# Optimization experiments

Measured on AMD Instinct MI355X. Metric: run time of the kernel, lower is better.

## Reference

```python
import jax, jax.numpy as jnp
import numpy as np

S = 8192          # past KV length
H = 4096          # hidden size
NH = 32           # heads
HD = 128          # head dim
INNER = 16384     # MLP inner (4h)
ROT = 64          # rotary dim per 2D-rope half
NUM_LAYERS = 28
LAYER_ID = 0
ALPHA = (2.0 * NUM_LAYERS) ** 0.5
QK_COEFF = float(LAYER_ID + 1)            # query_key_layer_scaling_coeff
COEFF = (128.0 ** 0.5) * QK_COEFF         # math.sqrt(128) * coeff
EPS = 1e-5


def layernorm(x, w, b):
    mu = jnp.mean(x, axis=-1, keepdims=True)
    var = jnp.var(x, axis=-1, keepdims=True)
    return (x - mu) * jax.lax.rsqrt(var + EPS) * w + b


def rotate_half(x):
    # x: [..., 64]; GLM rotate-half at 32
    return jnp.concatenate([-x[..., 32:], x[..., :32]], axis=-1)


def setup_inputs() -> dict:
    key = jax.random.key(0)
    ks = jax.random.split(key, 16)
    # rotary cache (as in the driver script)
    inv_freq = 1.0 / (10000.0 ** (jnp.arange(0, ROT, 2, dtype=jnp.float32) / ROT))  # [32]
    t = jnp.arange(512, dtype=jnp.float32)
    freqs = jnp.einsum('i,j->ij', t, inv_freq)          # [512,32]
    emb = jnp.concatenate([freqs, freqs], axis=-1)      # [512,64]
    w = lambda k, shp: jax.random.normal(k, shp, dtype=jnp.float32) * 0.02
    return {
        'hidden_states': jax.random.normal(ks[0], (1, H), dtype=jnp.float32),
        'past_key': jax.random.normal(ks[1], (S, NH, HD), dtype=jnp.float32),
        'past_value': jax.random.normal(ks[2], (S, NH, HD), dtype=jnp.float32),
        'cos_cached': jnp.cos(emb),
        'sin_cached': jnp.sin(emb),
        'ln1_w': jnp.ones((H,), jnp.float32), 'ln1_b': jnp.zeros((H,), jnp.float32),
        'qkv_w': w(ks[3], (3 * H, H)), 'qkv_b': w(ks[4], (3 * H,)),
        'dense_w': w(ks[5], (H, H)), 'dense_b': w(ks[6], (H,)),
        'ln2_w': jnp.ones((H,), jnp.float32), 'ln2_b': jnp.zeros((H,), jnp.float32),
        'fc1_w': w(ks[7], (INNER, H)), 'fc1_b': w(ks[8], (INNER,)),
        'fc2_w': w(ks[9], (H, INNER)), 'fc2_b': w(ks[10], (H,)),
        'position_ids': jax.random.randint(ks[11], (1, 1), 0, 512),
        'block_position_ids': jax.random.randint(ks[12], (1, 1), 0, 512),
        'attention_mask': jnp.zeros((1, 1, S + 1), dtype=bool),
    }


def reference(hidden_states, past_key, past_value, cos_cached, sin_cached,
              ln1_w, ln1_b, qkv_w, qkv_b, dense_w, dense_b,
              ln2_w, ln2_b, fc1_w, fc1_b, fc2_w, fc2_b,
              position_ids, block_position_ids, attention_mask):
    # rotary lookups: embedding then transpose(0,1) -> [q_len,1,64]
    pos_cos = jnp.transpose(cos_cached[position_ids], (1, 0, 2))
    pos_sin = jnp.transpose(sin_cached[position_ids], (1, 0, 2))
    blk_cos = jnp.transpose(cos_cached[block_position_ids], (1, 0, 2))
    blk_sin = jnp.transpose(sin_cached[block_position_ids], (1, 0, 2))

    residual = layernorm(hidden_states, ln1_w, ln1_b)          # [1, H]
    qkv = residual @ qkv_w.T + qkv_b                           # [1, 3H]
    qkv = qkv.reshape(-1, NH, 3 * HD)                          # [1, 32, 384]
    query, key_new, value_new = jnp.split(qkv, 3, axis=2)      # each [1,32,128]

    q1, q2 = jnp.split(query, 2, axis=2)                       # [1,32,64] each
    k1, k2 = jnp.split(key_new, 2, axis=2)
    q1 = q1 * pos_cos + rotate_half(q1) * pos_sin
    k1 = k1 * pos_cos + rotate_half(k1) * pos_sin
    q2 = q2 * blk_cos + rotate_half(q2) * blk_sin
    k2 = k2 * blk_cos + rotate_half(k2) * blk_sin
    q = jnp.concatenate([q1, q2], axis=-1)                     # [1,32,128]
    k_new = jnp.concatenate([k1, k2], axis=-1)                 # [1,32,128]

    k = jnp.concatenate([past_key, k_new], axis=0)             # [S+1,32,128]
    v = jnp.concatenate([past_value, value_new], axis=0)       # [S+1,32,128]

    # scores: [heads, q=1, S+1]
    scores = jnp.einsum('qhd,khd->hqk', q / COEFF, k)
    scores = jnp.where(attention_mask, jnp.float32(-10000.0), scores)
    scores = scores * QK_COEFF
    probs = jax.nn.softmax(scores, axis=-1)
    ctx = jnp.einsum('hqk,khd->qhd', probs, v).reshape(-1, H)  # [1,4096]

    attn_out = ctx @ dense_w.T + dense_b
    hidden = residual * ALPHA + attn_out

    residual2 = layernorm(hidden, ln2_w, ln2_b)
    mlp = jax.nn.gelu(residual2 @ fc1_w.T + fc1_b, approximate=True)
    mlp = mlp @ fc2_w.T + fc2_b
    out = residual2 * ALPHA + mlp
    return (out, k, v)
```

## Files before the change

### kernel.cpp

```cpp
#include <hip/hip_runtime.h>
#include <math.h>

#define S_PAST 8192
#define S_TOT  8193
#define HID    4096
#define NH     32
#define HD     128
#define INNER  16384
#define CH     16
#define NCH    512
#define S_PAD  8224
#define ALPHA_ 7.483314773547883f
#define INV_COEFF 0.08838834764831845f
#define EPS_ 1e-5f

__global__ __launch_bounds__(256) void ln_kernel(const float* __restrict__ xin,
                                                 const float* __restrict__ w,
                                                 const float* __restrict__ b,
                                                 float* __restrict__ out) {
    int tid = threadIdx.x;
    float xs[16];
    float s = 0.f, s2 = 0.f;
#pragma unroll
    for (int i = 0; i < 16; ++i) {
        float v = xin[tid + i * 256];
        xs[i] = v; s += v; s2 += v * v;
    }
    for (int off = 32; off; off >>= 1) {
        s  += __shfl_down(s, off, 64);
        s2 += __shfl_down(s2, off, 64);
    }
    __shared__ float rs[4], rs2[4];
    __shared__ float mu_s, ri_s;
    int wid = tid >> 6, lane = tid & 63;
    if (lane == 0) { rs[wid] = s; rs2[wid] = s2; }
    __syncthreads();
    if (tid == 0) {
        float S1 = rs[0] + rs[1] + rs[2] + rs[3];
        float S2 = rs2[0] + rs2[1] + rs2[2] + rs2[3];
        float mu = S1 / HID;
        float var = S2 / HID - mu * mu;
        mu_s = mu;
        ri_s = rsqrtf(var + EPS_);
    }
    __syncthreads();
    float mu = mu_s, ri = ri_s;
#pragma unroll
    for (int i = 0; i < 16; ++i) {
        int idx = tid + i * 256;
        out[idx] = (xs[i] - mu) * ri * w[idx] + b[idx];
    }
}

template <int C, int MODE>
__global__ __launch_bounds__(256) void gemv_kernel(
        const float* __restrict__ Wm, const float* __restrict__ bias,
        const float* __restrict__ x, float* __restrict__ y,
        const float* __restrict__ res) {
    int wid = threadIdx.x >> 6, lane = threadIdx.x & 63;
    int r = blockIdx.x * 4 + wid;
    const float4* __restrict__ rowv = (const float4*)(Wm + (size_t)r * C);
    const float4* __restrict__ xv = (const float4*)x;
    constexpr int IT = C / 4 / 64;
    float acc0 = 0.f, acc1 = 0.f;
#pragma unroll
    for (int it = 0; it < IT; it += 2) {
        float4 w0 = rowv[lane + it * 64];
        float4 x0 = xv[lane + it * 64];
        float4 w1 = rowv[lane + (it + 1) * 64];
        float4 x1 = xv[lane + (it + 1) * 64];
        acc0 += w0.x * x0.x + w0.y * x0.y + w0.z * x0.z + w0.w * x0.w;
        acc1 += w1.x * x1.x + w1.y * x1.y + w1.z * x1.z + w1.w * x1.w;
    }
    float acc = acc0 + acc1;
    for (int off = 32; off; off >>= 1) acc += __shfl_down(acc, off, 64);
    if (lane == 0) {
        float t = acc + bias[r];
        if (MODE == 1) t += ALPHA_ * res[r];
        if (MODE == 2) {
            float u = t;
            t = 0.5f * u * (1.f + tanhf(0.7978845608028654f * (u + 0.044715f * u * u * u)));
        }
        y[r] = t;
    }
}

__global__ __launch_bounds__(128) void rope_kv_kernel(
        const float* __restrict__ qkv, const float* __restrict__ cosc,
        const float* __restrict__ sinc, const int* __restrict__ pos_ids,
        const int* __restrict__ blk_ids, float* __restrict__ qrot,
        float* __restrict__ kout, float* __restrict__ vout) {
    int h = blockIdx.x, d = threadIdx.x;
    int pos = pos_ids[0], blk = blk_ids[0];
    const float* qh = qkv + h * 384;
    float q = qh[d], k = qh[128 + d], v = qh[256 + d];
    int half = d >> 6;
    int i = d & 63;
    int p = half ? blk : pos;
    float c = cosc[p * 64 + i];
    float s = sinc[p * 64 + i];
    float qpart, kpart;
    int base = half * 64;
    if (i < 32) { qpart = -qh[base + i + 32]; kpart = -qh[128 + base + i + 32]; }
    else        { qpart =  qh[base + i - 32]; kpart =  qh[128 + base + i - 32]; }
    float qo = q * c + qpart * s;
    float ko = k * c + kpart * s;
    qrot[h * HD + d] = qo * INV_COEFF;
    size_t o = (size_t)S_PAST * HID + h * HD + d;
    kout[o] = ko;
    vout[o] = v;
}

__global__ __launch_bounds__(512) void scores_kcopy(
        const float* __restrict__ qrot, const float* __restrict__ pastk,
        float* __restrict__ kout, const unsigned char* __restrict__ mask,
        float* __restrict__ probs, float* __restrict__ pL) {
    int tid = threadIdx.x;
    int t = tid & 255, u = tid >> 8;
    int s0 = blockIdx.x * CH;
    int rows = (blockIdx.x == NCH - 1) ? (S_TOT - s0) : CH;
    int rstart = u * 8;
    int rend = u ? rows : 8;
    int a = t >> 5;
    const float4* __restrict__ qv = (const float4*)qrot;
    float4 q0 = qv[t], q1 = qv[256 + t], q2 = qv[512 + t], q3 = qv[768 + t];
    __shared__ float sc[CH + 1][NH + 1];
#pragma unroll 4
    for (int r = rstart; r < rend; ++r) {
        int srow = s0 + r;
        const float* kbase = (srow < S_PAST) ? pastk : kout;
        const float4* krow = (const float4*)(kbase + (size_t)srow * HID);
        float4 k0 = krow[t], k1 = krow[256 + t];
        float4 k2 = krow[512 + t], k3 = krow[768 + t];
        if (srow < S_PAST) {
            float4* ko = (float4*)(kout + (size_t)srow * HID);
            ko[t] = k0; ko[256 + t] = k1; ko[512 + t] = k2; ko[768 + t] = k3;
        }
        float d0 = q0.x * k0.x + q0.y * k0.y + q0.z * k0.z + q0.w * k0.w;
        float d1 = q1.x * k1.x + q1.y * k1.y + q1.z * k1.z + q1.w * k1.w;
        float d2 = q2.x * k2.x + q2.y * k2.y + q2.z * k2.z + q2.w * k2.w;
        float d3 = q3.x * k3.x + q3.y * k3.y + q3.z * k3.z + q3.w * k3.w;
#pragma unroll
        for (int off = 1; off < 32; off <<= 1) {
            d0 += __shfl_xor(d0, off, 64);
            d1 += __shfl_xor(d1, off, 64);
            d2 += __shfl_xor(d2, off, 64);
            d3 += __shfl_xor(d3, off, 64);
        }
        if ((t & 31) == 0) {
            if (mask[srow]) { d0 = d1 = d2 = d3 = -10000.f; }
            sc[r][a]      = __expf(d0);
            sc[r][8 + a]  = __expf(d1);
            sc[r][16 + a] = __expf(d2);
            sc[r][24 + a] = __expf(d3);
        }
    }
    __syncthreads();
    for (int i = tid; i < rows * NH; i += 512) {
        int h = i & 31, r = i >> 5;
        probs[(size_t)h * S_PAD + s0 + r] = sc[r][h];
    }
    if (tid < 256) {
        int h = tid >> 3, j = tid & 7;
        float e = 0.f;
        for (int r = j; r < rows; r += 8) e += sc[r][h];
#pragma unroll
        for (int off = 1; off < 8; off <<= 1) e += __shfl_xor(e, off, 64);
        if (j == 0) pL[h * NCH + blockIdx.x] = e;
    }
}

__global__ __launch_bounds__(512) void pv_vcopy(
        const float* __restrict__ probs, const float* __restrict__ pastv,
        float* __restrict__ vout, float* __restrict__ pctx) {
    int tid = threadIdx.x;
    int t = tid & 255, u = tid >> 8;
    int s0 = blockIdx.x * CH;
    int rows = (blockIdx.x == NCH - 1) ? (S_TOT - s0) : CH;
    int rstart = u * 8;
    int rend = u ? rows : 8;
    int a = t >> 5;
    __shared__ float pl[NH][CH + 2];
    __shared__ float acc_lds[256][16];
    for (int i = tid; i < rows * NH; i += 512) {
        int h = i & 31, r = i >> 5;
        pl[h][r] = probs[(size_t)h * S_PAD + s0 + r];
    }
    __syncthreads();
    float4 a0 = {0,0,0,0}, a1 = {0,0,0,0}, a2 = {0,0,0,0}, a3 = {0,0,0,0};
#pragma unroll 4
    for (int r = rstart; r < rend; ++r) {
        int srow = s0 + r;
        const float* vbase = (srow < S_PAST) ? pastv : vout;
        const float4* vrow = (const float4*)(vbase + (size_t)srow * HID);
        float4 v0 = vrow[t], v1 = vrow[256 + t];
        float4 v2 = vrow[512 + t], v3 = vrow[768 + t];
        if (srow < S_PAST) {
            float4* vo = (float4*)(vout + (size_t)srow * HID);
            vo[t] = v0; vo[256 + t] = v1; vo[512 + t] = v2; vo[768 + t] = v3;
        }
        float p0 = pl[a][r], p1 = pl[8 + a][r], p2 = pl[16 + a][r], p3 = pl[24 + a][r];
        a0.x += p0 * v0.x; a0.y += p0 * v0.y; a0.z += p0 * v0.z; a0.w += p0 * v0.w;
        a1.x += p1 * v1.x; a1.y += p1 * v1.y; a1.z += p1 * v1.z; a1.w += p1 * v1.w;
        a2.x += p2 * v2.x; a2.y += p2 * v2.y; a2.z += p2 * v2.z; a2.w += p2 * v2.w;
        a3.x += p3 * v3.x; a3.y += p3 * v3.y; a3.z += p3 * v3.z; a3.w += p3 * v3.w;
    }
    if (u == 1) {
        acc_lds[t][0]  = a0.x; acc_lds[t][1]  = a0.y; acc_lds[t][2]  = a0.z; acc_lds[t][3]  = a0.w;
        acc_lds[t][4]  = a1.x; acc_lds[t][5]  = a1.y; acc_lds[t][6]  = a1.z; acc_lds[t][7]  = a1.w;
        acc_lds[t][8]  = a2.x; acc_lds[t][9]  = a2.y; acc_lds[t][10] = a2.z; acc_lds[t][11] = a2.w;
        acc_lds[t][12] = a3.x; acc_lds[t][13] = a3.y; acc_lds[t][14] = a3.z; acc_lds[t][15] = a3.w;
    }
    __syncthreads();
    if (u == 0) {
        a0.x += acc_lds[t][0];  a0.y += acc_lds[t][1];  a0.z += acc_lds[t][2];  a0.w += acc_lds[t][3];
        a1.x += acc_lds[t][4];  a1.y += acc_lds[t][5];  a1.z += acc_lds[t][6];  a1.w += acc_lds[t][7];
        a2.x += acc_lds[t][8];  a2.y += acc_lds[t][9];  a2.z += acc_lds[t][10]; a2.w += acc_lds[t][11];
        a3.x += acc_lds[t][12]; a3.y += acc_lds[t][13]; a3.z += acc_lds[t][14]; a3.w += acc_lds[t][15];
        float4* pc = (float4*)(pctx + (size_t)blockIdx.x * HID);
        pc[t] = a0; pc[256 + t] = a1; pc[512 + t] = a2; pc[768 + t] = a3;
    }
}

__global__ __launch_bounds__(256) void ctx_reduce1(const float* __restrict__ pctx,
                                                   const float* __restrict__ pL,
                                                   float* __restrict__ pctx2,
                                                   float* __restrict__ pL2) {
    int b = blockIdx.x, tid = threadIdx.x;
    float4 a0 = {0,0,0,0}, a1 = {0,0,0,0}, a2 = {0,0,0,0}, a3 = {0,0,0,0};
#pragma unroll
    for (int c = 0; c < 8; ++c) {
        const float4* row = (const float4*)(pctx + (size_t)(b * 8 + c) * HID);
        float4 v0 = row[tid], v1 = row[256 + tid], v2 = row[512 + tid], v3 = row[768 + tid];
        a0.x += v0.x; a0.y += v0.y; a0.z += v0.z; a0.w += v0.w;
        a1.x += v1.x; a1.y += v1.y; a1.z += v1.z; a1.w += v1.w;
        a2.x += v2.x; a2.y += v2.y; a2.z += v2.z; a2.w += v2.w;
        a3.x += v3.x; a3.y += v3.y; a3.z += v3.z; a3.w += v3.w;
    }
    float4* o = (float4*)(pctx2 + (size_t)b * HID);
    o[tid] = a0; o[256 + tid] = a1; o[512 + tid] = a2; o[768 + tid] = a3;
    if (tid < NH) {
        float s = 0.f;
#pragma unroll
        for (int c = 0; c < 8; ++c) s += pL[tid * NCH + b * 8 + c];
        pL2[tid * 64 + b] = s;
    }
}

__global__ __launch_bounds__(256) void ctx_reduce2(const float* __restrict__ pctx2,
                                                   const float* __restrict__ pL2,
                                                   float* __restrict__ ctx) {
    int tid = threadIdx.x;
    __shared__ float Lh[NH];
    if (tid < NH) {
        float s = 0.f;
        for (int j = 0; j < 64; ++j) s += pL2[tid * 64 + j];
        Lh[tid] = s;
    }
    __syncthreads();
    int idx = blockIdx.x * 256 + tid;
    float a = 0.f;
    for (int c = 0; c < 64; ++c) a += pctx2[(size_t)c * HID + idx];
    ctx[idx] = a / Lh[idx >> 7];
}

extern "C" void kernel_launch(void* const* d_in, const int* in_sizes, int n_in,
                              void* d_out, int out_size, void* d_ws, size_t ws_size,
                              hipStream_t stream) {
    const float* hidden = (const float*)d_in[0];
    const float* past_k = (const float*)d_in[1];
    const float* past_v = (const float*)d_in[2];
    const float* cosc = (const float*)d_in[3];
    const float* sinc = (const float*)d_in[4];
    const float* ln1w = (const float*)d_in[5];
    const float* ln1b = (const float*)d_in[6];
    const float* qkvw = (const float*)d_in[7];
    const float* qkvb = (const float*)d_in[8];
    const float* denw = (const float*)d_in[9];
    const float* denb = (const float*)d_in[10];
    const float* ln2w = (const float*)d_in[11];
    const float* ln2b = (const float*)d_in[12];
    const float* fc1w = (const float*)d_in[13];
    const float* fc1b = (const float*)d_in[14];
    const float* fc2w = (const float*)d_in[15];
    const float* fc2b = (const float*)d_in[16];
    const int* pos = (const int*)d_in[17];
    const int* blk = (const int*)d_in[18];
    const unsigned char* mask = (const unsigned char*)d_in[19];

    float* out_f = (float*)d_out;
    float* kout = out_f + HID;
    float* vout = kout + (size_t)S_TOT * HID;

    float* ws = (float*)d_ws;
    float* resid1 = ws;
    float* qkvv   = ws + 4096;
    float* qrot   = ws + 16384;
    float* ctx    = ws + 20480;
    float* hid2   = ws + 24576;
    float* resid2 = ws + 28672;
    float* mlpi   = ws + 32768;
    float* probs  = ws + 49152;
    float* pL     = ws + 312320;
    float* pL2    = ws + 328704;
    float* pctx   = ws + 330752;
    float* pctx2  = ws + 2427904;

    ln_kernel<<<1, 256, 0, stream>>>(hidden, ln1w, ln1b, resid1);
    gemv_kernel<HID, 0><<<3 * HID / 4, 256, 0, stream>>>(qkvw, qkvb, resid1, qkvv, nullptr);
    rope_kv_kernel<<<NH, HD, 0, stream>>>(qkvv, cosc, sinc, pos, blk, qrot, kout, vout);
    scores_kcopy<<<NCH, 512, 0, stream>>>(qrot, past_k, kout, mask, probs, pL);
    pv_vcopy<<<NCH, 512, 0, stream>>>(probs, past_v, vout, pctx);
    ctx_reduce1<<<64, 256, 0, stream>>>(pctx, pL, pctx2, pL2);
    ctx_reduce2<<<16, 256, 0, stream>>>(pctx2, pL2, ctx);
    gemv_kernel<HID, 1><<<HID / 4, 256, 0, stream>>>(denw, denb, ctx, hid2, resid1);
    ln_kernel<<<1, 256, 0, stream>>>(hid2, ln2w, ln2b, resid2);
    gemv_kernel<HID, 2><<<INNER / 4, 256, 0, stream>>>(fc1w, fc1b, resid2, mlpi, nullptr);
    gemv_kernel<INNER, 1><<<HID / 4, 256, 0, stream>>>(fc2w, fc2b, mlpi, out_f, resid2);
}
```

Baseline: 292.1 us.

## Fuse attention scores and PV passes into a single one-pass kernel

Merges the separate scores/K-copy and PV/V-copy kernels into one kernel where each thread computes exp scores in registers and immediately accumulates them against V rows, tracking per-head exp sums locally. This removes the intermediate probs buffer round trip through global memory and one kernel launch, and overlaps K and V streaming within each block. It also caps the gemv inner-loop unroll at 8. The fused loop carries more live registers per thread, which may reduce occupancy.

```diff
diff --git a/kernel.cpp b/kernel.cpp
--- a/kernel.cpp
+++ b/kernel.cpp
@@ -9,7 +9,6 @@
 #define INNER  16384
 #define CH     16
 #define NCH    512
-#define S_PAD  8224
 #define ALPHA_ 7.483314773547883f
 #define INV_COEFF 0.08838834764831845f
 #define EPS_ 1e-5f
@@ -63,7 +62,7 @@
     const float4* __restrict__ xv = (const float4*)x;
     constexpr int IT = C / 4 / 64;
     float acc0 = 0.f, acc1 = 0.f;
-#pragma unroll
+#pragma unroll 8
     for (int it = 0; it < IT; it += 2) {
         float4 w0 = rowv[lane + it * 64];
         float4 x0 = xv[lane + it * 64];
@@ -111,10 +110,11 @@
     vout[o] = v;
 }
 
-__global__ __launch_bounds__(512) void scores_kcopy(
+__global__ __launch_bounds__(512) void attn_onepass(
         const float* __restrict__ qrot, const float* __restrict__ pastk,
-        float* __restrict__ kout, const unsigned char* __restrict__ mask,
-        float* __restrict__ probs, float* __restrict__ pL) {
+        const float* __restrict__ pastv, float* __restrict__ kout,
+        float* __restrict__ vout, const unsigned char* __restrict__ mask,
+        float* __restrict__ pctx, float* __restrict__ pL) {
     int tid = threadIdx.x;
     int t = tid & 255, u = tid >> 8;
     int s0 = blockIdx.x * CH;
@@ -124,15 +124,17 @@
     int a = t >> 5;
     const float4* __restrict__ qv = (const float4*)qrot;
     float4 q0 = qv[t], q1 = qv[256 + t], q2 = qv[512 + t], q3 = qv[768 + t];
-    __shared__ float sc[CH + 1][NH + 1];
+    float4 a0 = {0,0,0,0}, a1 = {0,0,0,0}, a2 = {0,0,0,0}, a3 = {0,0,0,0};
+    float eL0 = 0.f, eL1 = 0.f, eL2 = 0.f, eL3 = 0.f;
 #pragma unroll 4
     for (int r = rstart; r < rend; ++r) {
         int srow = s0 + r;
-        const float* kbase = (srow < S_PAST) ? pastk : kout;
+        bool past = srow < S_PAST;
+        const float* kbase = past ? pastk : kout;
         const float4* krow = (const float4*)(kbase + (size_t)srow * HID);
         float4 k0 = krow[t], k1 = krow[256 + t];
         float4 k2 = krow[512 + t], k3 = krow[768 + t];
-        if (srow < S_PAST) {
+        if (past) {
             float4* ko = (float4*)(kout + (size_t)srow * HID);
             ko[t] = k0; ko[256 + t] = k1; ko[512 + t] = k2; ko[768 + t] = k3;
         }
@@ -147,69 +149,33 @@
             d2 += __shfl_xor(d2, off, 64);
             d3 += __shfl_xor(d3, off, 64);
         }
-        if ((t & 31) == 0) {
-            if (mask[srow]) { d0 = d1 = d2 = d3 = -10000.f; }
-            sc[r][a]      = __expf(d0);
-            sc[r][8 + a]  = __expf(d1);
-            sc[r][16 + a] = __expf(d2);
-            sc[r][24 + a] = __expf(d3);
-        }
-    }
-    __syncthreads();
-    for (int i = tid; i < rows * NH; i += 512) {
-        int h = i & 31, r = i >> 5;
-        probs[(size_t)h * S_PAD + s0 + r] = sc[r][h];
-    }
-    if (tid < 256) {
-        int h = tid >> 3, j = tid & 7;
-        float e = 0.f;
-        for (int r = j; r < rows; r += 8) e += sc[r][h];
-#pragma unroll
-        for (int off = 1; off < 8; off <<= 1) e += __shfl_xor(e, off, 64);
-        if (j == 0) pL[h * NCH + blockIdx.x] = e;
-    }
-}
-
-__global__ __launch_bounds__(512) void pv_vcopy(
-        const float* __restrict__ probs, const float* __restrict__ pastv,
-        float* __restrict__ vout, float* __restrict__ pctx) {
-    int tid = threadIdx.x;
-    int t = tid & 255, u = tid >> 8;
-    int s0 = blockIdx.x * CH;
-    int rows = (blockIdx.x == NCH - 1) ? (S_TOT - s0) : CH;
-    int rstart = u * 8;
-    int rend = u ? rows : 8;
-    int a = t >> 5;
-    __shared__ float pl[NH][CH + 2];
-    __shared__ float acc_lds[256][16];
-    for (int i = tid; i < rows * NH; i += 512) {
-        int h = i & 31, r = i >> 5;
-        pl[h][r] = probs[(size_t)h * S_PAD + s0 + r];
-    }
-    __syncthreads();
-    float4 a0 = {0,0,0,0}, a1 = {0,0,0,0}, a2 = {0,0,0,0}, a3 = {0,0,0,0};
-#pragma unroll 4
-    for (int r = rstart; r < rend; ++r) {
-        int srow = s0 + r;
-        const float* vbase = (srow < S_PAST) ? pastv : vout;
+        if (mask[srow]) { d0 = d1 = d2 = d3 = -10000.f; }
+        float p0 = __expf(d0), p1 = __expf(d1), p2 = __expf(d2), p3 = __expf(d3);
+        eL0 += p0; eL1 += p1; eL2 += p2; eL3 += p3;
+        const float* vbase = past ? pastv : vout;
         const float4* vrow = (const float4*)(vbase + (size_t)srow * HID);
         float4 v0 = vrow[t], v1 = vrow[256 + t];
         float4 v2 = vrow[512 + t], v3 = vrow[768 + t];
-        if (srow < S_PAST) {
+        if (past) {
             float4* vo = (float4*)(vout + (size_t)srow * HID);
             vo[t] = v0; vo[256 + t] = v1; vo[512 + t] = v2; vo[768 + t] = v3;
         }
-        float p0 = pl[a][r], p1 = pl[8 + a][r], p2 = pl[16 + a][r], p3 = pl[24 + a][r];
         a0.x += p0 * v0.x; a0.y += p0 * v0.y; a0.z += p0 * v0.z; a0.w += p0 * v0.w;
         a1.x += p1 * v1.x; a1.y += p1 * v1.y; a1.z += p1 * v1.z; a1.w += p1 * v1.w;
         a2.x += p2 * v2.x; a2.y += p2 * v2.y; a2.z += p2 * v2.z; a2.w += p2 * v2.w;
         a3.x += p3 * v3.x; a3.y += p3 * v3.y; a3.z += p3 * v3.z; a3.w += p3 * v3.w;
     }
+    __shared__ float acc_lds[256][16];
+    __shared__ float eLds[2][8][4];
     if (u == 1) {
         acc_lds[t][0]  = a0.x; acc_lds[t][1]  = a0.y; acc_lds[t][2]  = a0.z; acc_lds[t][3]  = a0.w;
         acc_lds[t][4]  = a1.x; acc_lds[t][5]  = a1.y; acc_lds[t][6]  = a1.z; acc_lds[t][7]  = a1.w;
         acc_lds[t][8]  = a2.x; acc_lds[t][9]  = a2.y; acc_lds[t][10] = a2.z; acc_lds[t][11] = a2.w;
         acc_lds[t][12] = a3.x; acc_lds[t][13] = a3.y; acc_lds[t][14] = a3.z; acc_lds[t][15] = a3.w;
+    }
+    if ((t & 31) == 0) {
+        eLds[u][a][0] = eL0; eLds[u][a][1] = eL1;
+        eLds[u][a][2] = eL2; eLds[u][a][3] = eL3;
     }
     __syncthreads();
     if (u == 0) {
@@ -219,6 +185,10 @@
         a3.x += acc_lds[t][12]; a3.y += acc_lds[t][13]; a3.z += acc_lds[t][14]; a3.w += acc_lds[t][15];
         float4* pc = (float4*)(pctx + (size_t)blockIdx.x * HID);
         pc[t] = a0; pc[256 + t] = a1; pc[512 + t] = a2; pc[768 + t] = a3;
+    }
+    if (tid < NH) {
+        int ah = tid & 7, g = tid >> 3;
+        pL[tid * NCH + blockIdx.x] = eLds[0][ah][g] + eLds[1][ah][g];
     }
 }
 
@@ -300,17 +270,15 @@
     float* hid2   = ws + 24576;
     float* resid2 = ws + 28672;
     float* mlpi   = ws + 32768;
-    float* probs  = ws + 49152;
-    float* pL     = ws + 312320;
-    float* pL2    = ws + 328704;
-    float* pctx   = ws + 330752;
-    float* pctx2  = ws + 2427904;
+    float* pL     = ws + 49152;
+    float* pL2    = ws + 65536;
+    float* pctx   = ws + 67584;
+    float* pctx2  = ws + 2164736;
 
     ln_kernel<<<1, 256, 0, stream>>>(hidden, ln1w, ln1b, resid1);
     gemv_kernel<HID, 0><<<3 * HID / 4, 256, 0, stream>>>(qkvw, qkvb, resid1, qkvv, nullptr);
     rope_kv_kernel<<<NH, HD, 0, stream>>>(qkvv, cosc, sinc, pos, blk, qrot, kout, vout);
-    scores_kcopy<<<NCH, 512, 0, stream>>>(qrot, past_k, kout, mask, probs, pL);
-    pv_vcopy<<<NCH, 512, 0, stream>>>(probs, past_v, vout, pctx);
+    attn_onepass<<<NCH, 512, 0, stream>>>(qrot, past_k, past_v, kout, vout, mask, pctx, pL);
     ctx_reduce1<<<64, 256, 0, stream>>>(pctx, pL, pctx2, pL2);
     ctx_reduce2<<<16, 256, 0, stream>>>(pctx2, pL2, ctx);
     gemv_kernel<HID, 1><<<HID / 4, 256, 0, stream>>>(denw, denb, ctx, hid2, resid1);
```

New measurement: 288.2 us. No clear change (-1.3%).
